# Optimization experiments

Hardware: AMD Instinct MI355X
Metric: run time of the kernel (lower is better)

Reference implementation:

```python
import jax, jax.numpy as jnp
import numpy as np

B = 4            # batch size (max batch index + 1, fixed by construction)
H, W = 176, 200  # feature_map_size; x in [0,H), y in [0,W)
C_IN, C_OUT = 128, 256
BW, N = 4096, 64
EPS = 1e-5       # torch LayerNorm default


def setup_inputs() -> dict:
    key = jax.random.key(0)
    k1, k2, k3, k4, k5, k6, k7 = jax.random.split(key, 7)
    window_features = jax.random.normal(k1, (BW, N, C_IN), jnp.float32)
    bidx = jax.random.randint(k2, (BW, N, 1), 0, B)
    xidx = jax.random.randint(k3, (BW, N, 1), -8, H + 8)   # includes invalid coords
    yidx = jax.random.randint(k4, (BW, N, 1), -8, W + 8)
    window_indices = jnp.concatenate([bidx, xidx, yidx], axis=-1).astype(jnp.int32)
    norm_weight = 1.0 + 0.1 * jax.random.normal(k5, (C_IN,), jnp.float32)
    norm_bias = 0.1 * jax.random.normal(k6, (C_IN,), jnp.float32)
    lin_weight = jax.random.normal(k7, (C_OUT, C_IN), jnp.float32) / np.sqrt(C_IN)
    return {"window_features": window_features, "window_indices": window_indices,
            "norm_weight": norm_weight, "norm_bias": norm_bias, "lin_weight": lin_weight}


def reference(window_features, window_indices, norm_weight, norm_bias, lin_weight):
    # window_features: (BW, N, C_IN); window_indices: (BW, N, 3) = (batch, x, y)
    bw, n, c = window_features.shape
    feats = window_features.reshape(-1, c)                # (P, C)
    idx = window_indices.reshape(-1, 3)
    b, x, y = idx[:, 0], idx[:, 1], idx[:, 2]
    valid = (x >= 0) & (x < H) & (y >= 0) & (y < W)

    # unique + index_add_ + sparse-to-dense == scatter-add into dense BEV grid.
    # Invalid rows are routed out-of-bounds and dropped.
    bs = jnp.where(valid, b, B)
    xs = jnp.where(valid, x, 0)
    ys = jnp.where(valid, y, 0)
    # dense layout matches spconv: spatial_shape=[W, H], indices (b, y, x)
    dense_sum = jnp.zeros((B, W, H, c), window_features.dtype)
    dense_sum = dense_sum.at[bs, ys, xs].add(feats, mode="drop")
    count = jnp.zeros((B, W, H), window_features.dtype)
    count = count.at[bs, ys, xs].add(1.0, mode="drop")
    occupied = count > 0                                   # cells holding a unique voxel

    # LayerNorm over C (patch_norm=True) then Linear (bias=False) on occupied cells
    mu = jnp.mean(dense_sum, axis=-1, keepdims=True)
    var = jnp.mean(jnp.square(dense_sum - mu), axis=-1, keepdims=True)
    normed = (dense_sum - mu) * jax.lax.rsqrt(var + EPS) * norm_weight + norm_bias
    dense_out = jnp.einsum("bwhc,oc->bwho", normed, lin_weight)
    dense_out = jnp.where(occupied[..., None], dense_out, 0.0)  # empty cells stay zero

    # gather_operation: pull dense features back to each valid window point
    gathered = dense_out[jnp.where(valid, b, 0), ys, xs]   # (P, C_OUT)
    new_feats = jnp.where(valid[:, None], gathered, 0.0).reshape(bw, n, C_OUT)
    return new_feats, window_indices
```

## Files before the change

kernel.cpp:

```cpp
#include <hip/hip_runtime.h>
#include <stdint.h>

#define HH 176
#define WW 200
#define BB 4
#define CIN 128
#define COUT 256
#define NPTS (4096 * 64)
#define CELLS (BB * WW * HH)
#define FEAT_OUT_ELEMS ((size_t)NPTS * COUT)
#define CAP 32
#define LDSW 260

typedef __attribute__((ext_vector_type(8))) short bf16x8;
typedef __attribute__((ext_vector_type(4))) float f32x4;

__device__ __forceinline__ unsigned short f2bf(float f) {
    union { float f; unsigned int u; } c; c.f = f;
    unsigned int u = c.u;
    u += 0x7fffu + ((u >> 16) & 1u);
    return (unsigned short)(u >> 16);
}

__global__ __launch_bounds__(256) void build_kernel(
    const int* __restrict__ idx, int* __restrict__ counts, int* __restrict__ plist,
    float* __restrict__ out_idx)
{
    int p = blockIdx.x * 256 + threadIdx.x;
    int b = idx[3 * p], x = idx[3 * p + 1], y = idx[3 * p + 2];
    out_idx[3 * p]     = (float)b;
    out_idx[3 * p + 1] = (float)x;
    out_idx[3 * p + 2] = (float)y;
    if ((unsigned)x < HH && (unsigned)y < WW) {
        int cell = (b * WW + y) * HH + x;
        int slot = atomicAdd(&counts[cell], 1);
        if (slot < CAP) plist[(size_t)cell * CAP + slot] = p;
    }
}

__global__ __launch_bounds__(256) void zero_invalid_kernel(
    const int* __restrict__ idx, float* __restrict__ out_feats)
{
    int p = blockIdx.x * 4 + (threadIdx.x >> 6);
    int lane = threadIdx.x & 63;
    int x = idx[3 * p + 1], y = idx[3 * p + 2];
    if (!((unsigned)x < HH && (unsigned)y < WW)) {
        float4 z = { 0.0f, 0.0f, 0.0f, 0.0f };
        *(float4*)(out_feats + (size_t)p * COUT + lane * 4) = z;
    }
}

__global__ __launch_bounds__(256) void cell_kernel(
    const float* __restrict__ feats, const int* __restrict__ counts,
    const int* __restrict__ plist,
    const float* __restrict__ nw, const float* __restrict__ nb,
    unsigned short* __restrict__ normed)
{
    int cell = blockIdx.x * 4 + (threadIdx.x >> 6);
    int lane = threadIdx.x & 63;
    int n = counts[cell]; n = n < CAP ? n : CAP;
    const int* pl = plist + (size_t)cell * CAP;
    float a0 = 0.0f, a1 = 0.0f;
    for (int i = 0; i < n; ++i) {
        int pid = pl[i];
        float2 v = *(const float2*)(feats + (size_t)pid * CIN + lane * 2);
        a0 += v.x; a1 += v.y;
    }
    float s = a0 + a1;
    float ss = a0 * a0 + a1 * a1;
    #pragma unroll
    for (int m = 32; m >= 1; m >>= 1) {
        s  += __shfl_xor(s, m, 64);
        ss += __shfl_xor(ss, m, 64);
    }
    float mu  = s * (1.0f / 128.0f);
    float var = ss * (1.0f / 128.0f) - mu * mu;
    float inv = rsqrtf(var + 1e-5f);
    float w0 = nw[lane * 2], w1 = nw[lane * 2 + 1];
    float b0 = nb[lane * 2], b1 = nb[lane * 2 + 1];
    ushort2 st;
    st.x = f2bf((a0 - mu) * inv * w0 + b0);
    st.y = f2bf((a1 - mu) * inv * w1 + b1);
    *(ushort2*)(normed + (size_t)cell * CIN + lane * 2) = st;
}

__global__ __launch_bounds__(256) void wcvt_kernel(
    const float* __restrict__ lw, unsigned short* __restrict__ wb)
{
    int i = blockIdx.x * 256 + threadIdx.x;
    wb[i] = f2bf(lw[i]);
}

__global__ __launch_bounds__(256) void gemm_scatter_kernel(
    const unsigned short* __restrict__ A,
    const unsigned short* __restrict__ Wb,
    const int* __restrict__ counts,
    const int* __restrict__ plist,
    float* __restrict__ out)
{
    __shared__ float lds_out[16 * LDSW];
    __shared__ int scnt[64];
    __shared__ int spid[64 * CAP];

    int n0 = blockIdx.x * 64;
    int tid = threadIdx.x;
    int w = tid >> 6;
    int lane = tid & 63;
    int l15 = lane & 15;
    int kgrp = (lane >> 4) * 8;
    int orow = (lane >> 4) * 4;

    if (tid < 64) {
        int cnt = counts[n0 + tid]; cnt = cnt < CAP ? cnt : CAP;
        scnt[tid] = cnt;
        for (int s = 0; s < cnt; ++s)
            spid[tid * CAP + s] = plist[(size_t)(n0 + tid) * CAP + s];
    }

    bf16x8 a[4][4];
    #pragma unroll
    for (int i = 0; i < 4; ++i)
        #pragma unroll
        for (int kk = 0; kk < 4; ++kk)
            a[i][kk] = *(const bf16x8*)(Wb + (size_t)(((w * 4 + i) * 16 + l15) * CIN) + kgrp + kk * 32);

    const unsigned short* bbase = A + (size_t)(n0 + l15) * CIN + kgrp;
    bf16x8 bcur[4];
    #pragma unroll
    for (int kk = 0; kk < 4; ++kk)
        bcur[kk] = *(const bf16x8*)(bbase + kk * 32);

    __syncthreads();

    #pragma unroll
    for (int j = 0; j < 4; ++j) {
        bf16x8 bnext[4];
        if (j < 3) {
            #pragma unroll
            for (int kk = 0; kk < 4; ++kk)
                bnext[kk] = *(const bf16x8*)(bbase + (size_t)(j + 1) * 16 * CIN + kk * 32);
        } else {
            #pragma unroll
            for (int kk = 0; kk < 4; ++kk) bnext[kk] = bcur[kk];
        }

        f32x4 acc[4];
        #pragma unroll
        for (int i = 0; i < 4; ++i) acc[i] = (f32x4){0.0f, 0.0f, 0.0f, 0.0f};
        #pragma unroll
        for (int kk = 0; kk < 4; ++kk)
            #pragma unroll
            for (int i = 0; i < 4; ++i)
                acc[i] = __builtin_amdgcn_mfma_f32_16x16x32_bf16(a[i][kk], bcur[kk], acc[i], 0, 0, 0);

        #pragma unroll
        for (int i = 0; i < 4; ++i)
            *(f32x4*)(&lds_out[l15 * LDSW + (w * 4 + i) * 16 + orow]) = acc[i];

        __syncthreads();

        int cbase = j * 16;
        for (int c = 0; c < 16; ++c) {
            int cnt = scnt[cbase + c];
            const float* row = &lds_out[c * LDSW];
            for (int t = 0; t < cnt; ++t) {
                int pid = spid[(cbase + c) * CAP + t];
                out[(size_t)pid * COUT + tid] = row[tid];
            }
        }

        __syncthreads();

        #pragma unroll
        for (int kk = 0; kk < 4; ++kk) bcur[kk] = bnext[kk];
    }
}

extern "C" void kernel_launch(void* const* d_in, const int* in_sizes, int n_in,
                              void* d_out, int out_size, void* d_ws, size_t ws_size,
                              hipStream_t stream)
{
    const float* feats = (const float*)d_in[0];
    const int*   idx   = (const int*)d_in[1];
    const float* nw    = (const float*)d_in[2];
    const float* nb    = (const float*)d_in[3];
    const float* lw    = (const float*)d_in[4];
    float* out = (float*)d_out;

    char* ws = (char*)d_ws;
    int* counts = (int*)ws;
    int* plist  = (int*)(ws + (1u << 20));
    unsigned short* normed = (unsigned short*)(ws + (20u << 20));
    unsigned short* wb     = (unsigned short*)(ws + (60u << 20));

    hipMemsetAsync(counts, 0, (size_t)CELLS * 4, stream);
    zero_invalid_kernel<<<NPTS / 4, 256, 0, stream>>>(idx, out);
    build_kernel<<<NPTS / 256, 256, 0, stream>>>(idx, counts, plist, out + FEAT_OUT_ELEMS);
    cell_kernel<<<CELLS / 4, 256, 0, stream>>>(feats, counts, plist, nw, nb, normed);
    wcvt_kernel<<<COUT * CIN / 256, 256, 0, stream>>>(lw, wb);
    gemm_scatter_kernel<<<CELLS / 64, 256, 0, stream>>>(normed, wb, counts, plist, out);
}
```

Before: 503.5 us.

## Fuse invalid-row zeroing into build and flatten bf16-staged GEMM scatter

Removes the separate zero_invalid kernel by having build_kernel zero invalid output rows after recording validity in shared memory. The GEMM kernel now computes all four 16-cell tiles first, stores results as bf16 in LDS, then scatters via a flattened (point, cell) list so each wave writes whole rows with float4 stores. This removes per-tile barriers and serial per-cell scatter loops at the cost of bf16 rounding of outputs and dropping the B-operand prefetch.

```diff
diff --git a/kernel.cpp b/kernel.cpp
--- a/kernel.cpp
+++ b/kernel.cpp
@@ -10,7 +10,8 @@
 #define CELLS (BB * WW * HH)
 #define FEAT_OUT_ELEMS ((size_t)NPTS * COUT)
 #define CAP 32
-#define LDSW 260
+#define LDSW16 260
+#define FLATCAP 1024
 
 typedef __attribute__((ext_vector_type(8))) short bf16x8;
 typedef __attribute__((ext_vector_type(4))) float f32x4;
@@ -21,33 +22,36 @@
     u += 0x7fffu + ((u >> 16) & 1u);
     return (unsigned short)(u >> 16);
 }
+__device__ __forceinline__ float bf2f(unsigned int h16) {
+    union { unsigned int u; float f; } c; c.u = h16 << 16;
+    return c.f;
+}
 
 __global__ __launch_bounds__(256) void build_kernel(
     const int* __restrict__ idx, int* __restrict__ counts, int* __restrict__ plist,
-    float* __restrict__ out_idx)
-{
-    int p = blockIdx.x * 256 + threadIdx.x;
+    float* __restrict__ out_idx, float* __restrict__ out_feats)
+{
+    __shared__ unsigned char validf[256];
+    int tid = threadIdx.x;
+    int p0 = blockIdx.x * 256;
+    int p = p0 + tid;
     int b = idx[3 * p], x = idx[3 * p + 1], y = idx[3 * p + 2];
     out_idx[3 * p]     = (float)b;
     out_idx[3 * p + 1] = (float)x;
     out_idx[3 * p + 2] = (float)y;
-    if ((unsigned)x < HH && (unsigned)y < WW) {
+    bool valid = ((unsigned)x < HH && (unsigned)y < WW);
+    validf[tid] = valid ? 1 : 0;
+    if (valid) {
         int cell = (b * WW + y) * HH + x;
         int slot = atomicAdd(&counts[cell], 1);
         if (slot < CAP) plist[(size_t)cell * CAP + slot] = p;
     }
-}
-
-__global__ __launch_bounds__(256) void zero_invalid_kernel(
-    const int* __restrict__ idx, float* __restrict__ out_feats)
-{
-    int p = blockIdx.x * 4 + (threadIdx.x >> 6);
-    int lane = threadIdx.x & 63;
-    int x = idx[3 * p + 1], y = idx[3 * p + 2];
-    if (!((unsigned)x < HH && (unsigned)y < WW)) {
-        float4 z = { 0.0f, 0.0f, 0.0f, 0.0f };
-        *(float4*)(out_feats + (size_t)p * COUT + lane * 4) = z;
-    }
+    __syncthreads();
+    int w = tid >> 6, lane = tid & 63;
+    float4 z = { 0.0f, 0.0f, 0.0f, 0.0f };
+    for (int v = w; v < 256; v += 4)
+        if (!validf[v])
+            *(float4*)(out_feats + (size_t)(p0 + v) * COUT + lane * 4) = z;
 }
 
 __global__ __launch_bounds__(256) void cell_kernel(
@@ -98,9 +102,10 @@
     const int* __restrict__ plist,
     float* __restrict__ out)
 {
-    __shared__ float lds_out[16 * LDSW];
-    __shared__ int scnt[64];
-    __shared__ int spid[64 * CAP];
+    __shared__ unsigned short lds16[64 * LDSW16];
+    __shared__ int fpid[FLATCAP];
+    __shared__ unsigned char fcell[FLATCAP];
+    __shared__ int nflat;
 
     int n0 = blockIdx.x * 64;
     int tid = threadIdx.x;
@@ -110,11 +115,21 @@
     int kgrp = (lane >> 4) * 8;
     int orow = (lane >> 4) * 4;
 
+    if (tid == 0) nflat = 0;
+    __syncthreads();
+
     if (tid < 64) {
         int cnt = counts[n0 + tid]; cnt = cnt < CAP ? cnt : CAP;
-        scnt[tid] = cnt;
-        for (int s = 0; s < cnt; ++s)
-            spid[tid * CAP + s] = plist[(size_t)(n0 + tid) * CAP + s];
+        if (cnt > 0) {
+            int base = atomicAdd(&nflat, cnt);
+            for (int s = 0; s < cnt; ++s) {
+                int pos = base + s;
+                if (pos < FLATCAP) {
+                    fpid[pos] = plist[(size_t)(n0 + tid) * CAP + s];
+                    fcell[pos] = (unsigned char)tid;
+                }
+            }
+        }
     }
 
     bf16x8 a[4][4];
@@ -125,24 +140,13 @@
             a[i][kk] = *(const bf16x8*)(Wb + (size_t)(((w * 4 + i) * 16 + l15) * CIN) + kgrp + kk * 32);
 
     const unsigned short* bbase = A + (size_t)(n0 + l15) * CIN + kgrp;
-    bf16x8 bcur[4];
-    #pragma unroll
-    for (int kk = 0; kk < 4; ++kk)
-        bcur[kk] = *(const bf16x8*)(bbase + kk * 32);
-
-    __syncthreads();
 
     #pragma unroll
     for (int j = 0; j < 4; ++j) {
-        bf16x8 bnext[4];
-        if (j < 3) {
-            #pragma unroll
-            for (int kk = 0; kk < 4; ++kk)
-                bnext[kk] = *(const bf16x8*)(bbase + (size_t)(j + 1) * 16 * CIN + kk * 32);
-        } else {
-            #pragma unroll
-            for (int kk = 0; kk < 4; ++kk) bnext[kk] = bcur[kk];
-        }
+        bf16x8 bb[4];
+        #pragma unroll
+        for (int kk = 0; kk < 4; ++kk)
+            bb[kk] = *(const bf16x8*)(bbase + (size_t)j * 16 * CIN + kk * 32);
 
         f32x4 acc[4];
         #pragma unroll
@@ -151,28 +155,33 @@
         for (int kk = 0; kk < 4; ++kk)
             #pragma unroll
             for (int i = 0; i < 4; ++i)
-                acc[i] = __builtin_amdgcn_mfma_f32_16x16x32_bf16(a[i][kk], bcur[kk], acc[i], 0, 0, 0);
-
-        #pragma unroll
-        for (int i = 0; i < 4; ++i)
-            *(f32x4*)(&lds_out[l15 * LDSW + (w * 4 + i) * 16 + orow]) = acc[i];
-
-        __syncthreads();
-
-        int cbase = j * 16;
-        for (int c = 0; c < 16; ++c) {
-            int cnt = scnt[cbase + c];
-            const float* row = &lds_out[c * LDSW];
-            for (int t = 0; t < cnt; ++t) {
-                int pid = spid[(cbase + c) * CAP + t];
-                out[(size_t)pid * COUT + tid] = row[tid];
-            }
+                acc[i] = __builtin_amdgcn_mfma_f32_16x16x32_bf16(a[i][kk], bb[kk], acc[i], 0, 0, 0);
+
+        #pragma unroll
+        for (int i = 0; i < 4; ++i) {
+            int o = (w * 4 + i) * 16 + orow;
+            ushort4 st;
+            st.x = f2bf(acc[i][0]);
+            st.y = f2bf(acc[i][1]);
+            st.z = f2bf(acc[i][2]);
+            st.w = f2bf(acc[i][3]);
+            *(ushort4*)(&lds16[(j * 16 + l15) * LDSW16 + o]) = st;
         }
-
-        __syncthreads();
-
-        #pragma unroll
-        for (int kk = 0; kk < 4; ++kk) bcur[kk] = bnext[kk];
+    }
+
+    __syncthreads();
+
+    int nt = nflat; nt = nt < FLATCAP ? nt : FLATCAP;
+    for (int k = w; k < nt; k += 4) {
+        int pid = fpid[k];
+        int c = fcell[k];
+        ushort4 v = *(const ushort4*)(&lds16[c * LDSW16 + lane * 4]);
+        float4 o4;
+        o4.x = bf2f(v.x);
+        o4.y = bf2f(v.y);
+        o4.z = bf2f(v.z);
+        o4.w = bf2f(v.w);
+        *(float4*)(out + (size_t)pid * COUT + lane * 4) = o4;
     }
 }
 
@@ -194,8 +203,7 @@
     unsigned short* wb     = (unsigned short*)(ws + (60u << 20));
 
     hipMemsetAsync(counts, 0, (size_t)CELLS * 4, stream);
-    zero_invalid_kernel<<<NPTS / 4, 256, 0, stream>>>(idx, out);
-    build_kernel<<<NPTS / 256, 256, 0, stream>>>(idx, counts, plist, out + FEAT_OUT_ELEMS);
+    build_kernel<<<NPTS / 256, 256, 0, stream>>>(idx, counts, plist, out + FEAT_OUT_ELEMS, out);
     cell_kernel<<<CELLS / 4, 256, 0, stream>>>(feats, counts, plist, nw, nb, normed);
     wcvt_kernel<<<COUT * CIN / 256, 256, 0, stream>>>(lw, wb);
     gemm_scatter_kernel<<<CELLS / 64, 256, 0, stream>>>(normed, wb, counts, plist, out);
```

After: 478.2 us. -5.0%, faster.
